# Kernel optimization log

Hardware: AMD Instinct MI355X
Metric: run time of the kernel (lower is better)

## Reference

```python
import jax, jax.numpy as jnp
import numpy as np

S, B, I, H = 256, 512, 46, 256  # seqlen, batch, i_dim, h_dim
EPS = 1e-5


def setup_inputs() -> dict:
    key = jax.random.key(0)
    ks = iter(jax.random.split(key, 64))
    nrm = lambda shape, s=0.05: jax.random.normal(next(ks), shape, dtype=jnp.float32) * s
    inp = {}
    inp['X'] = jax.random.normal(next(ks), (S, B, I), dtype=jnp.float32)
    inp['M'] = (jax.random.uniform(next(ks), (S, B, I)) > 0.5).astype(jnp.float32)
    inp['mask'] = (jax.random.uniform(next(ks), (S, B)) > 0.1).astype(jnp.float32)
    C = I - 6  # 40 clinical channels
    inp['i2h_w'] = nrm((H, 6)); inp['i2h_b'] = nrm((H,))
    inp['comb_w'] = nrm((C, 2 * C)); inp['comb_b'] = nrm((C,))
    inp['down_w'] = nrm((H, C)); inp['down_b'] = nrm((H,))
    inp['conv1_w'] = nrm((H, C)); inp['conv1_b'] = nrm((H,))
    inp['conv2_w'] = nrm((H, H)); inp['conv2_b'] = nrm((H,))
    inp['bn1_g'] = jnp.ones((H,), jnp.float32); inp['bn1_b'] = jnp.zeros((H,), jnp.float32)
    inp['bn2_g'] = jnp.ones((H,), jnp.float32); inp['bn2_b'] = jnp.zeros((H,), jnp.float32)
    for p in ('r1', 'r2'):
        inp[p + '_wih'] = nrm((3 * H, H)); inp[p + '_whh'] = nrm((3 * H, H))
        inp[p + '_bih'] = nrm((3 * H,)); inp[p + '_bhh'] = nrm((3 * H,))
        inp[p + '_cw'] = nrm((H, 2 * H)); inp[p + '_cb'] = nrm((H,))
    inp['ln1_g'] = jnp.ones((H,), jnp.float32); inp['ln1_b'] = jnp.zeros((H,), jnp.float32)
    inp['ln2_g'] = jnp.ones((H,), jnp.float32); inp['ln2_b'] = jnp.zeros((H,), jnp.float32)
    inp['ln3_g'] = jnp.ones((8,), jnp.float32); inp['ln3_b'] = jnp.zeros((8,), jnp.float32)
    inp['nn1_w'] = nrm((8, H)); inp['nn1_b'] = nrm((8,))
    inp['nn2_w'] = nrm((2, 8)); inp['nn2_b'] = nrm((2,))
    return inp


def _bn(x, g, b):
    # BatchNorm1d in training mode: stats over (seq, batch) per channel, biased var
    mu = x.mean((0, 1))
    var = x.var((0, 1))
    return (x - mu) * jax.lax.rsqrt(var + EPS) * g + b


def _ln(x, g, b):
    mu = x.mean(-1, keepdims=True)
    var = x.var(-1, keepdims=True)
    return (x - mu) * jax.lax.rsqrt(var + EPS) * g + b


def _modgru(Xs, h0, mask, wih, whh, bih, bhh, cw, cb):
    # precompute input-gate projections for all timesteps: [S,B,3H]
    gi = jnp.einsum('sbi,gi->sbg', Xs, wih) + bih

    def step(h, inp):
        x, g, m = inp  # x:[B,H], g:[B,3H], m:[B]
        gh = h @ whh.T + bhh
        ir, iz, inn = jnp.split(g, 3, axis=-1)
        hr, hz, hn = jnp.split(gh, 3, axis=-1)
        r = jax.nn.sigmoid(ir + hr)
        z = jax.nn.sigmoid(iz + hz)
        n = jnp.tanh(inn + r * hn)
        h_new = (1.0 - z) * n + z * h  # GRUCell update
        mm = m[:, None]
        h = h_new * mm + h * (1.0 - mm)  # mask blend
        out = jnp.concatenate([x, h], axis=-1) @ cw.T + cb  # com2
        return h, out

    _, outs = jax.lax.scan(step, h0, (Xs, gi, mask))
    return outs


def reference(X, M, mask, i2h_w, i2h_b, comb_w, comb_b, down_w, down_b,
              conv1_w, conv1_b, conv2_w, conv2_b, bn1_g, bn1_b, bn2_g, bn2_b,
              r1_wih, r1_whh, r1_bih, r1_bhh, r1_cw, r1_cb,
              r2_wih, r2_whh, r2_bih, r2_bhh, r2_cw, r2_cb,
              ln1_g, ln1_b, ln2_g, ln2_b, ln3_g, ln3_b,
              nn1_w, nn1_b, nn2_w, nn2_b):
    p_info = X[0, :, -6:]          # [B,6] static patient info
    Xin = X[:, :, :-6]             # [S,B,40]
    Min = M[:, :, :-6]
    h0 = p_info @ i2h_w.T + i2h_b  # [B,H]
    res = Xin @ down_w.T + down_b  # [S,B,H]
    Xc = jnp.concatenate([Xin, Min], axis=-1) @ comb_w.T + comb_b
    # kernel-size-1 convs == per-timestep linear (layout kept [S,B,C])
    out = Xc @ conv1_w.T + conv1_b
    out = jax.nn.relu(_bn(out, bn1_g, bn1_b))
    out = out @ conv2_w.T + conv2_b
    out = _bn(out, bn2_g, bn2_b)
    hx = out + res
    hx = _ln(_modgru(hx, h0, mask, r1_wih, r1_whh, r1_bih, r1_bhh, r1_cw, r1_cb), ln1_g, ln1_b)
    hx = _ln(_modgru(hx, h0, mask, r2_wih, r2_whh, r2_bih, r2_bhh, r2_cw, r2_cb), ln2_g, ln2_b)
    hx = jax.nn.relu(hx @ nn1_w.T + nn1_b)
    hx = _ln(hx, ln3_g, ln3_b)
    return hx @ nn2_w.T + nn2_b  # [S,B,2]
```

## Files before the change

### kernel.cpp

```cpp
#include <hip/hip_runtime.h>
#include <hip/hip_bf16.h>

#define SS 256
#define BB 512
#define II 46
#define HH 256
#define CC 40
#define SB (SS*BB)
#define G3 (3*HH)
#define EPSF 1e-5f
#define NPART (SB/64)

typedef __attribute__((ext_vector_type(8))) short bf16x8;
typedef __attribute__((ext_vector_type(4))) float f32x4;

__device__ __forceinline__ unsigned short f2bf_rne(float f){
  unsigned u = __float_as_uint(f);
  unsigned r = (u + 0x7FFFu + ((u >> 16) & 1u)) >> 16;
  return (unsigned short)r;
}
__device__ __forceinline__ float bf2f(unsigned short b){
  return __uint_as_float(((unsigned)b) << 16);
}
__device__ __forceinline__ void cvt8(const float* v, bf16x8& hi, bf16x8& lo){
  #pragma unroll
  for (int e=0;e<8;e++){
    unsigned short hb = f2bf_rne(v[e]);
    hi[e] = (short)hb;
    lo[e] = (short)f2bf_rne(v[e] - bf2f(hb));
  }
}

__global__ void split_w_k(const float* __restrict__ w, unsigned short* __restrict__ wh,
                          unsigned short* __restrict__ wl, int n){
  int i = blockIdx.x*256 + threadIdx.x;
  if (i >= n) return;
  float v = w[i];
  unsigned short hb = f2bf_rne(v);
  wh[i] = hb;
  wl[i] = f2bf_rne(v - bf2f(hb));
}

__global__ void h0_k(const float* __restrict__ X, const float* __restrict__ w,
                     const float* __restrict__ bias, float* __restrict__ h1c,
                     float* __restrict__ h2c){
  int b = blockIdx.x, jj = threadIdx.x;
  const float* p = X + (long long)b*II + (II - 6);
  float acc = bias[jj];
  #pragma unroll
  for (int c2=0;c2<6;c2++) acc = fmaf(p[c2], w[jj*6 + c2], acc);
  h1c[(long long)b*HH + jj] = acc;
  h2c[(long long)b*HH + jj] = acc;
}

__global__ void whht_bf_k(const float* __restrict__ w, unsigned short* __restrict__ wt){
  int idx = blockIdx.x*blockDim.x + threadIdx.x;
  if (idx >= G3*HH) return;
  int u = idx / HH, k = idx - u*HH;
  wt[(size_t)k*G3 + u] = f2bf_rne(w[idx]);
}

template<int MODE, int XM>
__global__ void gemm_tn(const float* __restrict__ A, int lda,
                        const float* __restrict__ W, int ldw,
                        const float* __restrict__ bias,
                        float* __restrict__ Co, int ldc,
                        int Mrows, int N, int K,
                        const float* __restrict__ A2, long long r0)
{
  __shared__ __align__(16) float As[32][132];
  __shared__ __align__(16) float Ws[32][132];
  const int m0 = blockIdx.x*128, n0 = blockIdx.y*128;
  const int t  = threadIdx.x;
  const int tm = t >> 4, tn = t & 15;
  float acc[8][8];
  #pragma unroll
  for (int i=0;i<8;i++)
    #pragma unroll
    for (int j2=0;j2<8;j2++) acc[i][j2] = 0.f;

  for (int k0=0;k0<K;k0+=32){
    #pragma unroll
    for (int u=0;u<16;u++){
      int idx = u*256 + t;
      int r = idx >> 5, c = idx & 31;
      int gk = k0 + c;
      float av = 0.f, wv = 0.f;
      if (gk < K){
        int gm = m0 + r;
        if (gm < Mrows){
          if (XM){
            long long gr = r0 + gm;
            av = (gk < CC) ? A[gr*II + gk] : A2[gr*II + (gk - CC)];
          } else {
            av = A[(long long)gm*lda + gk];
          }
        }
        int gn = n0 + r;
        if (gn < N)     wv = W[(long long)gn*ldw + gk];
      }
      As[c][r] = av;
      Ws[c][r] = wv;
    }
    __syncthreads();
    #pragma unroll
    for (int kk=0;kk<32;kk++){
      const float4 a0 = *(const float4*)&As[kk][tm*8];
      const float4 a1 = *(const float4*)&As[kk][tm*8+4];
      const float4 b0 = *(const float4*)&Ws[kk][tn*8];
      const float4 b1 = *(const float4*)&Ws[kk][tn*8+4];
      const float av[8] = {a0.x,a0.y,a0.z,a0.w,a1.x,a1.y,a1.z,a1.w};
      const float bv[8] = {b0.x,b0.y,b0.z,b0.w,b1.x,b1.y,b1.z,b1.w};
      #pragma unroll
      for (int i=0;i<8;i++)
        #pragma unroll
        for (int j2=0;j2<8;j2++) acc[i][j2] = fmaf(av[i], bv[j2], acc[i][j2]);
    }
    __syncthreads();
  }
  #pragma unroll
  for (int i=0;i<8;i++){
    int gm = m0 + tm*8 + i;
    if (gm < Mrows){
      #pragma unroll
      for (int j2=0;j2<8;j2++){
        int gn = n0 + tn*8 + j2;
        if (gn < N){
          long long oi = (long long)gm*ldc + gn;
          float val = acc[i][j2] + bias[gn];
          if (MODE == 1) val = fmaxf(val, 0.f);
          if (MODE == 2) val += Co[oi];
          Co[oi] = val;
        }
      }
    }
  }
}

__global__ void gemm_tn_dual2(const float* __restrict__ Xb, long long r0,
                              const float* __restrict__ W1, const float* __restrict__ b1,
                              float* __restrict__ Co1,
                              const float* __restrict__ A2, const float* __restrict__ W2,
                              const float* __restrict__ b2, float* __restrict__ Co2,
                              int Mrows)
{
  __shared__ __align__(16) float As1[32][132];
  __shared__ __align__(16) float As2[32][132];
  __shared__ __align__(16) float Ws1[32][132];
  __shared__ __align__(16) float Ws2[32][132];
  const int m0 = blockIdx.x*128, n0 = blockIdx.y*128;
  const int t  = threadIdx.x;
  const int tm = t >> 4, tn = t & 15;
  float acc1[8][8], acc2[8][8];
  #pragma unroll
  for (int i=0;i<8;i++)
    #pragma unroll
    for (int j2=0;j2<8;j2++){ acc1[i][j2] = 0.f; acc2[i][j2] = 0.f; }

  for (int k0=0;k0<CC;k0+=32){
    #pragma unroll
    for (int u=0;u<16;u++){
      int idx = u*256 + t;
      int r = idx >> 5, c = idx & 31;
      int gk = k0 + c;
      float a1=0.f, a2=0.f, w1=0.f, w2=0.f;
      if (gk < CC){
        int gm = m0 + r;
        if (gm < Mrows){
          long long gr = r0 + gm;
          a1 = Xb[gr*II + gk];
          a2 = A2[(long long)gm*CC + gk];
        }
        int gn = n0 + r;
        w1 = W1[(long long)gn*CC + gk];
        w2 = W2[(long long)gn*CC + gk];
      }
      As1[c][r] = a1; As2[c][r] = a2;
      Ws1[c][r] = w1; Ws2[c][r] = w2;
    }
    __syncthreads();
    #pragma unroll
    for (int kk=0;kk<32;kk++){
      const float4 p0 = *(const float4*)&As1[kk][tm*8];
      const float4 p1 = *(const float4*)&As1[kk][tm*8+4];
      const float4 q0 = *(const float4*)&As2[kk][tm*8];
      const float4 q1 = *(const float4*)&As2[kk][tm*8+4];
      const float4 u0 = *(const float4*)&Ws1[kk][tn*8];
      const float4 u1 = *(const float4*)&Ws1[kk][tn*8+4];
      const float4 v0 = *(const float4*)&Ws2[kk][tn*8];
      const float4 v1 = *(const float4*)&Ws2[kk][tn*8+4];
      const float a1v[8] = {p0.x,p0.y,p0.z,p0.w,p1.x,p1.y,p1.z,p1.w};
      const float a2v[8] = {q0.x,q0.y,q0.z,q0.w,q1.x,q1.y,q1.z,q1.w};
      const float w1v[8] = {u0.x,u0.y,u0.z,u0.w,u1.x,u1.y,u1.z,u1.w};
      const float w2v[8] = {v0.x,v0.y,v0.z,v0.w,v1.x,v1.y,v1.z,v1.w};
      #pragma unroll
      for (int i=0;i<8;i++)
        #pragma unroll
        for (int j2=0;j2<8;j2++){
          acc1[i][j2] = fmaf(a1v[i], w1v[j2], acc1[i][j2]);
          acc2[i][j2] = fmaf(a2v[i], w2v[j2], acc2[i][j2]);
        }
    }
    __syncthreads();
  }
  #pragma unroll
  for (int i=0;i<8;i++){
    int gm = m0 + tm*8 + i;
    if (gm < Mrows){
      #pragma unroll
      for (int j2=0;j2<8;j2++){
        int gn = n0 + tn*8 + j2;
        long long oi = (long long)gm*HH + gn;
        Co1[oi] = acc1[i][j2] + b1[gn];
        Co2[oi] = fmaxf(acc2[i][j2] + b2[gn], 0.f);
      }
    }
  }
}

template<int MODE>
__global__ __launch_bounds__(256) void gemm_mfp(
    const float* __restrict__ A, int lda,
    const unsigned short* __restrict__ Wh, const unsigned short* __restrict__ Wl, int ldw,
    const float* __restrict__ bias,
    float* __restrict__ Co, int ldc,
    int N, int K)
{
  __shared__ __align__(16) unsigned short Ah[128*32];
  __shared__ __align__(16) unsigned short Al[128*32];
  __shared__ __align__(16) unsigned short Bh[128*32];
  __shared__ __align__(16) unsigned short Bl[128*32];
  const int t = threadIdx.x;
  const int m0 = blockIdx.x*128, n0 = blockIdx.y*128;
  const int lane = t & 63, w = t >> 6;
  const int wm = (w & 1)*64, wn = (w >> 1)*64;
  const int fr = lane & 15, fg = lane >> 4;

  f32x4 acc[4][4];
  #pragma unroll
  for (int i=0;i<4;i++)
    #pragma unroll
    for (int j=0;j<4;j++){ f32x4 z; z[0]=0;z[1]=0;z[2]=0;z[3]=0; acc[i][j]=z; }

  for (int k0=0; k0<K; k0+=32){
    #pragma unroll
    for (int cc=0; cc<2; cc++){
      const int c   = t + cc*256;
      const int row = c >> 2, kg = c & 3;
      const int byte = row*64 + ((kg*16) ^ (((row>>1)&3)<<4));
      {
        const float* ap = A + (size_t)(m0+row)*lda + k0 + kg*8;
        float v[8];
        *(float4*)&v[0] = *(const float4*)ap;
        *(float4*)&v[4] = *(const float4*)(ap+4);
        bf16x8 hi, lo; cvt8(v, hi, lo);
        *(bf16x8*)((char*)Ah + byte) = hi;
        *(bf16x8*)((char*)Al + byte) = lo;
      }
      {
        const size_t off = (size_t)(n0+row)*ldw + k0 + kg*8;
        *(bf16x8*)((char*)Bh + byte) = *(const bf16x8*)&Wh[off];
        *(bf16x8*)((char*)Bl + byte) = *(const bf16x8*)&Wl[off];
      }
    }
    __syncthreads();
    bf16x8 ahi[4], alo[4], bhi[4], blo[4];
    #pragma unroll
    for (int mt=0; mt<4; mt++){
      const int r = wm + mt*16 + fr;
      const int byte = r*64 + ((fg*16) ^ (((r>>1)&3)<<4));
      ahi[mt] = *(const bf16x8*)((const char*)Ah + byte);
      alo[mt] = *(const bf16x8*)((const char*)Al + byte);
    }
    #pragma unroll
    for (int nt=0; nt<4; nt++){
      const int r = wn + nt*16 + fr;
      const int byte = r*64 + ((fg*16) ^ (((r>>1)&3)<<4));
      bhi[nt] = *(const bf16x8*)((const char*)Bh + byte);
      blo[nt] = *(const bf16x8*)((const char*)Bl + byte);
    }
    #pragma unroll
    for (int mt=0; mt<4; mt++)
      #pragma unroll
      for (int nt=0; nt<4; nt++){
        acc[mt][nt] = __builtin_amdgcn_mfma_f32_16x16x32_bf16(alo[mt], bhi[nt], acc[mt][nt], 0,0,0);
        acc[mt][nt] = __builtin_amdgcn_mfma_f32_16x16x32_bf16(ahi[mt], blo[nt], acc[mt][nt], 0,0,0);
        acc[mt][nt] = __builtin_amdgcn_mfma_f32_16x16x32_bf16(ahi[mt], bhi[nt], acc[mt][nt], 0,0,0);
      }
    __syncthreads();
  }

  #pragma unroll
  for (int mt=0; mt<4; mt++){
    #pragma unroll
    for (int nt=0; nt<4; nt++){
      const int col = n0 + wn + nt*16 + fr;
      const float bv = bias[col];
      #pragma unroll
      for (int i=0;i<4;i++){
        const int row = m0 + wm + mt*16 + fg*4 + i;
        const size_t oi = (size_t)row*ldc + col;
        float val = acc[mt][nt][i] + bv;
        if (MODE == 2) val += Co[oi];
        Co[oi] = val;
      }
    }
  }
}

__global__ __launch_bounds__(256) void gemm_mfp_dual(
    const float* __restrict__ A1, const float* __restrict__ A2,
    const unsigned short* __restrict__ Wh, const unsigned short* __restrict__ Wl,
    const float* __restrict__ bias,
    float* __restrict__ Co, int ldc, int N)
{
  __shared__ __align__(16) unsigned short Ah[128*32];
  __shared__ __align__(16) unsigned short Al[128*32];
  __shared__ __align__(16) unsigned short Bh[128*32];
  __shared__ __align__(16) unsigned short Bl[128*32];
  const int t = threadIdx.x;
  const int m0 = blockIdx.x*128, n0 = blockIdx.y*128;
  const int lane = t & 63, w = t >> 6;
  const int wm = (w & 1)*64, wn = (w >> 1)*64;
  const int fr = lane & 15, fg = lane >> 4;

  f32x4 acc[4][4];
  #pragma unroll
  for (int i=0;i<4;i++)
    #pragma unroll
    for (int j=0;j<4;j++){ f32x4 z; z[0]=0;z[1]=0;z[2]=0;z[3]=0; acc[i][j]=z; }

  for (int k0=0; k0<2*HH; k0+=32){
    const float* Abase = (k0 < HH) ? A1 : A2;
    const int    kofs  = (k0 < HH) ? k0 : (k0 - HH);
    #pragma unroll
    for (int cc=0; cc<2; cc++){
      const int c   = t + cc*256;
      const int row = c >> 2, kg = c & 3;
      const int byte = row*64 + ((kg*16) ^ (((row>>1)&3)<<4));
      {
        const float* ap = Abase + (size_t)(m0+row)*HH + kofs + kg*8;
        float v[8];
        *(float4*)&v[0] = *(const float4*)ap;
        *(float4*)&v[4] = *(const float4*)(ap+4);
        bf16x8 hi, lo; cvt8(v, hi, lo);
        *(bf16x8*)((char*)Ah + byte) = hi;
        *(bf16x8*)((char*)Al + byte) = lo;
      }
      {
        const size_t off = (size_t)(n0+row)*(2*HH) + k0 + kg*8;
        *(bf16x8*)((char*)Bh + byte) = *(const bf16x8*)&Wh[off];
        *(bf16x8*)((char*)Bl + byte) = *(const bf16x8*)&Wl[off];
      }
    }
    __syncthreads();
    bf16x8 ahi[4], alo[4], bhi[4], blo[4];
    #pragma unroll
    for (int mt=0; mt<4; mt++){
      const int r = wm + mt*16 + fr;
      const int byte = r*64 + ((fg*16) ^ (((r>>1)&3)<<4));
      ahi[mt] = *(const bf16x8*)((const char*)Ah + byte);
      alo[mt] = *(const bf16x8*)((const char*)Al + byte);
    }
    #pragma unroll
    for (int nt=0; nt<4; nt++){
      const int r = wn + nt*16 + fr;
      const int byte = r*64 + ((fg*16) ^ (((r>>1)&3)<<4));
      bhi[nt] = *(const bf16x8*)((const char*)Bh + byte);
      blo[nt] = *(const bf16x8*)((const char*)Bl + byte);
    }
    #pragma unroll
    for (int mt=0; mt<4; mt++)
      #pragma unroll
      for (int nt=0; nt<4; nt++){
        acc[mt][nt] = __builtin_amdgcn_mfma_f32_16x16x32_bf16(alo[mt], bhi[nt], acc[mt][nt], 0,0,0);
        acc[mt][nt] = __builtin_amdgcn_mfma_f32_16x16x32_bf16(ahi[mt], blo[nt], acc[mt][nt], 0,0,0);
        acc[mt][nt] = __builtin_amdgcn_mfma_f32_16x16x32_bf16(ahi[mt], bhi[nt], acc[mt][nt], 0,0,0);
      }
    __syncthreads();
  }

  #pragma unroll
  for (int mt=0; mt<4; mt++){
    #pragma unroll
    for (int nt=0; nt<4; nt++){
      const int col = n0 + wn + nt*16 + fr;
      const float bv = bias[col];
      #pragma unroll
      for (int i=0;i<4;i++){
        const int row = m0 + wm + mt*16 + fg*4 + i;
        const size_t oi = (size_t)row*ldc + col;
        Co[oi] = acc[mt][nt][i] + bv;
      }
    }
  }
}

__global__ void bn_partial_k(const float* __restrict__ Xc, float* __restrict__ ps,
                             float* __restrict__ pq, int pblk0){
  int blk = blockIdx.x, t = threadIdx.x;
  long long base = (long long)blk*64*HH;
  float s = 0.f, q = 0.f;
  for (int r=0;r<64;r++){
    float v = Xc[base + (long long)r*HH + t];
    s += v; q = fmaf(v, v, q);
  }
  ps[(size_t)(pblk0+blk)*HH + t] = s;
  pq[(size_t)(pblk0+blk)*HH + t] = q;
}

__global__ void bn_final_k(const float* __restrict__ ps, const float* __restrict__ pq,
                           const float* __restrict__ g, const float* __restrict__ b,
                           float* __restrict__ sc, float* __restrict__ sh){
  int t = threadIdx.x;
  double s = 0.0, q = 0.0;
  for (int i=0;i<NPART;i++){ s += (double)ps[(size_t)i*HH + t]; q += (double)pq[(size_t)i*HH + t]; }
  double mu  = s / (double)SB;
  double var = q / (double)SB - mu*mu;
  float scv = (float)((double)g[t] / sqrt(var + 1e-5));
  sc[t] = scv;
  sh[t] = (float)((double)b[t] - mu*(double)scv);
}

__global__ void fold_k(const float* __restrict__ w, const float* __restrict__ b,
                       const float* __restrict__ sc, const float* __restrict__ sh,
                       float* __restrict__ wf, float* __restrict__ bf, int K){
  int idx = blockIdx.x*blockDim.x + threadIdx.x;
  if (idx < 256*K){ int o = idx / K; wf[idx] = w[idx]*sc[o]; }
  if (idx < 256)  bf[idx] = b[idx]*sc[idx] + sh[idx];
}

__global__ void ln_rows_k(const float* __restrict__ Xi, float* __restrict__ Xo,
                          const float* __restrict__ g, const float* __restrict__ b){
  long long row = blockIdx.x;
  int t = threadIdx.x;
  float v = Xi[row*HH + t];
  float s = v, q = v*v;
  #pragma unroll
  for (int o=32;o>0;o>>=1){ s += __shfl_down(s,o); q += __shfl_down(q,o); }
  __shared__ float ssm[4], qqm[4];
  int w = t >> 6;
  if ((t & 63) == 0){ ssm[w] = s; qqm[w] = q; }
  __syncthreads();
  if (t == 0){ ssm[0] = ssm[0]+ssm[1]+ssm[2]+ssm[3]; qqm[0] = qqm[0]+qqm[1]+qqm[2]+qqm[3]; }
  __syncthreads();
  s = ssm[0]; q = qqm[0];
  float mu  = s * (1.f/HH);
  float var = q * (1.f/HH) - mu*mu;
  float rs  = rsqrtf(var + EPSF);
  Xo[row*HH + t] = (v - mu)*rs*g[t] + b[t];
}

#define DOT4(hv,A0,A1,A2,A3) \
  A0=fmaf(hv.x,w0.x,A0); A0=fmaf(hv.y,w1.x,A0); A0=fmaf(hv.z,w2.x,A0); A0=fmaf(hv.w,w3.x,A0); \
  A1=fmaf(hv.x,w0.y,A1); A1=fmaf(hv.y,w1.y,A1); A1=fmaf(hv.z,w2.y,A1); A1=fmaf(hv.w,w3.y,A1); \
  A2=fmaf(hv.x,w0.z,A2); A2=fmaf(hv.y,w1.z,A2); A2=fmaf(hv.z,w2.z,A2); A2=fmaf(hv.w,w3.z,A2); \
  A3=fmaf(hv.x,w0.w,A3); A3=fmaf(hv.y,w1.w,A3); A3=fmaf(hv.z,w2.w,A3); A3=fmaf(hv.w,w3.w,A3);

#define LDW_BF(dst, ofs) { \
  const uint2 u_ = *(const uint2*)(wbase + (size_t)(ofs)*G3); \
  dst.x = __uint_as_float(u_.x << 16); \
  dst.y = __uint_as_float(u_.x & 0xffff0000u); \
  dst.z = __uint_as_float(u_.y << 16); \
  dst.w = __uint_as_float(u_.y & 0xffff0000u); }

__global__ __launch_bounds__(768) void gru_scan_fused_k(
  const float* __restrict__ gi1, const unsigned short* __restrict__ w1T,
  const float* __restrict__ b1v, const float* __restrict__ m1v,
  float* __restrict__ hc1, float* __restrict__ Hh1o, int nst1,
  const float* __restrict__ gi2, const unsigned short* __restrict__ w2T,
  const float* __restrict__ b2v, const float* __restrict__ m2v,
  float* __restrict__ hc2, float* __restrict__ Hh2o, int nst2)
{
  const int gsel = blockIdx.x & 1;
  const int blk  = blockIdx.x >> 1;
  const float* gi    = gsel ? gi2 : gi1;
  const unsigned short* whhT = gsel ? w2T : w1T;
  const float* bhh   = gsel ? b2v : b1v;
  const float* mask0 = gsel ? m2v : m1v;
  float* hcar        = gsel ? hc2 : hc1;
  float* Hh          = gsel ? Hh2o : Hh1o;
  const int nst      = gsel ? nst2 : nst1;
  if (nst <= 0) return;

  const int t  = threadIdx.x;
  const int b0 = blk*4;
  const int cg = t % 192;
  const int ks = t / 192;
  const int c0 = cg*4;
  const int k0 = ks*64;
  __shared__ __align__(16) float h[4][260];
  __shared__ __align__(16) float part[4][4][776];
  __shared__ float mkz[4];

  const int uj = t & 255;
  const int ur = t >> 8;
  if (t < 512){
    h[ur  ][uj] = hcar[(size_t)(b0+ur  )*HH + uj];
    h[ur+2][uj] = hcar[(size_t)(b0+ur+2)*HH + uj];
  }
  float br=0.f, bz=0.f, bn_=0.f;
  if (t < 512){ br = bhh[uj]; bz = bhh[uj+HH]; bn_ = bhh[uj+2*HH]; }
  __syncthreads();

  const unsigned short* wbase = whhT + (size_t)k0*G3 + c0;

  for (int st=0; st<nst; ++st){
    float i0r=0,i0z=0,i0n=0, i1r=0,i1z=0,i1n=0;
    if (t < 512){
      const size_t ga = ((size_t)st*BB + b0 + ur  )*G3 + uj;
      const size_t gb = ((size_t)st*BB + b0 + ur+2)*G3 + uj;
      i0r=gi[ga]; i0z=gi[ga+HH]; i0n=gi[ga+2*HH];
      i1r=gi[gb]; i1z=gi[gb+HH]; i1n=gi[gb+2*HH];
    }
    if (t < 4) mkz[t] = mask0[(size_t)st*BB + b0 + t];

    float a00=0,a01=0,a02=0,a03=0;
    float a10=0,a11=0,a12=0,a13=0;
    float a20=0,a21=0,a22=0,a23=0;
    float a30=0,a31=0,a32=0,a33=0;
    #pragma unroll 4
    for (int kk=0; kk<64; kk+=4){
      float4 w0, w1, w2, w3;
      LDW_BF(w0, kk  );
      LDW_BF(w1, kk+1);
      LDW_BF(w2, kk+2);
      LDW_BF(w3, kk+3);
      const float4 h0 = *(const float4*)&h[0][k0+kk];
      const float4 h1 = *(const float4*)&h[1][k0+kk];
      const float4 h2 = *(const float4*)&h[2][k0+kk];
      const float4 h3 = *(const float4*)&h[3][k0+kk];
      DOT4(h0,a00,a01,a02,a03);
      DOT4(h1,a10,a11,a12,a13);
      DOT4(h2,a20,a21,a22,a23);
      DOT4(h3,a30,a31,a32,a33);
    }
    *(float4*)&part[ks][0][c0] = make_float4(a00,a01,a02,a03);
    *(float4*)&part[ks][1][c0] = make_float4(a10,a11,a12,a13);
    *(float4*)&part[ks][2][c0] = make_float4(a20,a21,a22,a23);
    *(float4*)&part[ks][3][c0] = make_float4(a30,a31,a32,a33);
    __syncthreads();

    if (t < 512){
      {
        const int r_ = ur;
        const float ar = part[0][r_][uj]+part[1][r_][uj]+part[2][r_][uj]+part[3][r_][uj] + br;
        const float az = part[0][r_][uj+HH]+part[1][r_][uj+HH]+part[2][r_][uj+HH]+part[3][r_][uj+HH] + bz;
        const float an = part[0][r_][uj+2*HH]+part[1][r_][uj+2*HH]+part[2][r_][uj+2*HH]+part[3][r_][uj+2*HH] + bn_;
        const float rr = 1.f/(1.f + __expf(-(i0r + ar)));
        const float zz = 1.f/(1.f + __expf(-(i0z + az)));
        const float nn = tanhf(fmaf(rr, an, i0n));
        const float hold = h[r_][uj];
        const float m = mkz[r_];
        const float hnew = (1.f - zz)*nn + zz*hold;
        const float hv = hnew*m + hold*(1.f - m);
        h[r_][uj] = hv;
        Hh[((size_t)st*BB + b0 + r_)*HH + uj] = hv;
      }
      {
        const int r_ = ur + 2;
        const float ar = part[0][r_][uj]+part[1][r_][uj]+part[2][r_][uj]+part[3][r_][uj] + br;
        const float az = part[0][r_][uj+HH]+part[1][r_][uj+HH]+part[2][r_][uj+HH]+part[3][r_][uj+HH] + bz;
        const float an = part[0][r_][uj+2*HH]+part[1][r_][uj+2*HH]+part[2][r_][uj+2*HH]+part[3][r_][uj+2*HH] + bn_;
        const float rr = 1.f/(1.f + __expf(-(i1r + ar)));
        const float zz = 1.f/(1.f + __expf(-(i1z + az)));
        const float nn = tanhf(fmaf(rr, an, i1n));
        const float hold = h[r_][uj];
        const float m = mkz[r_];
        const float hnew = (1.f - zz)*nn + zz*hold;
        const float hv = hnew*m + hold*(1.f - m);
        h[r_][uj] = hv;
        Hh[((size_t)st*BB + b0 + r_)*HH + uj] = hv;
      }
    }
    __syncthreads();
  }
  if (t < 512){
    hcar[(size_t)(b0+ur  )*HH + uj] = h[ur  ][uj];
    hcar[(size_t)(b0+ur+2)*HH + uj] = h[ur+2][uj];
  }
}

__global__ void head_ln_k(const float* __restrict__ hx,
                          const float* __restrict__ g2, const float* __restrict__ b2,
                          const float* __restrict__ w1, const float* __restrict__ b1,
                          const float* __restrict__ g3, const float* __restrict__ b3,
                          const float* __restrict__ w2, const float* __restrict__ b2h,
                          float* __restrict__ outp, long long r0){
  long long row = blockIdx.x;
  int t = threadIdx.x;
  float v = hx[row*HH + t];
  float s = v, q = v*v;
  #pragma unroll
  for (int o=32;o>0;o>>=1){ s += __shfl_down(s,o); q += __shfl_down(q,o); }
  __shared__ float ssm[4], qqm[4];
  int w = t >> 6;
  if ((t & 63) == 0){ ssm[w] = s; qqm[w] = q; }
  __syncthreads();
  if (t == 0){ ssm[0] = ssm[0]+ssm[1]+ssm[2]+ssm[3]; qqm[0] = qqm[0]+qqm[1]+qqm[2]+qqm[3]; }
  __syncthreads();
  s = ssm[0]; q = qqm[0];
  float mu  = s * (1.f/HH);
  float var = q * (1.f/HH) - mu*mu;
  float rs  = rsqrtf(var + EPSF);
  __shared__ float xs[HH];
  xs[t] = (v - mu)*rs*g2[t] + b2[t];
  __syncthreads();
  int o = t >> 5, l = t & 31;
  const float* wv = w1 + o*HH;
  float acc = 0.f;
  for (int k=l;k<HH;k+=32) acc = fmaf(xs[k], wv[k], acc);
  #pragma unroll
  for (int d=16;d>0;d>>=1) acc += __shfl_down(acc, d, 32);
  __shared__ float a8[8];
  if (l == 0) a8[o] = fmaxf(acc + b1[o], 0.f);
  __syncthreads();
  if (t == 0){
    float ss = 0.f;
    #pragma unroll
    for (int i=0;i<8;i++) ss += a8[i];
    float m8 = ss*0.125f;
    float qq = 0.f;
    #pragma unroll
    for (int i=0;i<8;i++){ float d = a8[i]-m8; qq = fmaf(d,d,qq); }
    float r8 = rsqrtf(qq*0.125f + EPSF);
    float y0 = b2h[0], y1 = b2h[1];
    #pragma unroll
    for (int i=0;i<8;i++){
      float vv = (a8[i]-m8)*r8*g3[i] + b3[i];
      y0 = fmaf(vv, w2[i],   y0);
      y1 = fmaf(vv, w2[8+i], y1);
    }
    outp[(r0+row)*2+0] = y0; outp[(r0+row)*2+1] = y1;
  }
}

extern "C" void kernel_launch(void* const* d_in, const int* in_sizes, int n_in,
                              void* d_out, int out_size, void* d_ws, size_t ws_size,
                              hipStream_t stream) {
  const float* X      = (const float*)d_in[0];
  const float* Mi     = (const float*)d_in[1];
  const float* mask   = (const float*)d_in[2];
  const float* i2h_w  = (const float*)d_in[3];
  const float* i2h_b  = (const float*)d_in[4];
  const float* comb_w = (const float*)d_in[5];
  const float* comb_b = (const float*)d_in[6];
  const float* down_w = (const float*)d_in[7];
  const float* down_b = (const float*)d_in[8];
  const float* conv1_w= (const float*)d_in[9];
  const float* conv1_b= (const float*)d_in[10];
  const float* conv2_w= (const float*)d_in[11];
  const float* conv2_b= (const float*)d_in[12];
  const float* bn1_g  = (const float*)d_in[13];
  const float* bn1_b  = (const float*)d_in[14];
  const float* bn2_g  = (const float*)d_in[15];
  const float* bn2_b  = (const float*)d_in[16];
  const float* r1_wih = (const float*)d_in[17];
  const float* r1_whh = (const float*)d_in[18];
  const float* r1_bih = (const float*)d_in[19];
  const float* r1_bhh = (const float*)d_in[20];
  const float* r1_cw  = (const float*)d_in[21];
  const float* r1_cb  = (const float*)d_in[22];
  const float* r2_wih = (const float*)d_in[23];
  const float* r2_whh = (const float*)d_in[24];
  const float* r2_bih = (const float*)d_in[25];
  const float* r2_bhh = (const float*)d_in[26];
  const float* r2_cw  = (const float*)d_in[27];
  const float* r2_cb  = (const float*)d_in[28];
  const float* ln1_g  = (const float*)d_in[29];
  const float* ln1_b  = (const float*)d_in[30];
  const float* ln2_g  = (const float*)d_in[31];
  const float* ln2_b  = (const float*)d_in[32];
  const float* ln3_g  = (const float*)d_in[33];
  const float* ln3_b  = (const float*)d_in[34];
  const float* nn1_w  = (const float*)d_in[35];
  const float* nn1_b  = (const float*)d_in[36];
  const float* nn2_w  = (const float*)d_in[37];
  const float* nn2_b  = (const float*)d_in[38];
  float* outp = (float*)d_out;

  const size_t us_elems = 2*((size_t)HH*HH + (size_t)HH*HH + (size_t)G3*HH
                           + (size_t)G3*HH + (size_t)HH*2*HH + (size_t)HH*2*HH)
                        + 2*(size_t)G3*HH;
  const size_t tail_floats = 2*(size_t)BB*HH + 2*(size_t)NPART*HH + 2*HH
                           + (size_t)256*40 + 256 + (size_t)HH*HH + 256
                           + (size_t)SB*CC
                           + (us_elems + 1)/2;
  int cands[6] = {256,128,64,32,16,8};
  int sc_chunk = 0;
  for (int ci=0; ci<6; ci++){
    size_t R = (size_t)512*cands[ci];
    size_t need = (R*2560 + tail_floats)*sizeof(float);
    if (need <= ws_size && R*2560 >= (size_t)SB*HH){ sc_chunk = cands[ci]; break; }
  }
  if (!sc_chunk) return;

  const size_t R = (size_t)512*sc_chunk;
  const int Ri = (int)R;
  const int nchunks = SB / Ri;

  float* wsf = (float*)d_ws;
  float* A   = wsf;
  float* GI1 = A + R*HH;
  float* Cxp = GI1;
  float* GI2 = GI1 + R*G3;
  float* Ee  = GI2 + R*G3;
  float* Hh2 = Ee + R*HH;
  float* Hx1 = Hh2 + R*HH;
  float* tl  = Hx1 + R*HH;
  float* H1C = tl;
  float* H2C = H1C + (size_t)BB*HH;
  float* PS  = H2C + (size_t)BB*HH;
  float* PQ  = PS  + (size_t)NPART*HH;
  float* SCv = PQ  + (size_t)NPART*HH;
  float* SHv = SCv + HH;
  float* W1F = SHv + HH;
  float* B1F = W1F + (size_t)256*40;
  float* W2F = B1F + HH;
  float* B2F = W2F + (size_t)HH*HH;
  float* XcF = B2F + HH;
  unsigned short* usb = (unsigned short*)(XcF + (size_t)SB*CC);
  unsigned short* C2H  = usb;
  unsigned short* C2L  = C2H  + (size_t)HH*HH;
  unsigned short* W2FH = C2L  + (size_t)HH*HH;
  unsigned short* W2FL = W2FH + (size_t)HH*HH;
  unsigned short* WI1H = W2FL + (size_t)HH*HH;
  unsigned short* WI1L = WI1H + (size_t)G3*HH;
  unsigned short* WI2H = WI1L + (size_t)G3*HH;
  unsigned short* WI2L = WI2H + (size_t)G3*HH;
  unsigned short* CW1H = WI2L + (size_t)G3*HH;
  unsigned short* CW1L = CW1H + (size_t)HH*2*HH;
  unsigned short* CW2H = CW1L + (size_t)HH*2*HH;
  unsigned short* CW2L = CW2H + (size_t)HH*2*HH;
  unsigned short* W1Tb = CW2L + (size_t)HH*2*HH;
  unsigned short* W2Tb = W1Tb + (size_t)HH*G3;

  whht_bf_k<<<(G3*HH + 255)/256, 256, 0, stream>>>(r1_whh, W1Tb);
  whht_bf_k<<<(G3*HH + 255)/256, 256, 0, stream>>>(r2_whh, W2Tb);
  split_w_k<<<(HH*HH + 255)/256, 256, 0, stream>>>(conv2_w, C2H, C2L, HH*HH);
  split_w_k<<<(G3*HH + 255)/256, 256, 0, stream>>>(r1_wih, WI1H, WI1L, G3*HH);
  split_w_k<<<(G3*HH + 255)/256, 256, 0, stream>>>(r2_wih, WI2H, WI2L, G3*HH);
  split_w_k<<<(HH*2*HH + 255)/256, 256, 0, stream>>>(r1_cw, CW1H, CW1L, HH*2*HH);
  split_w_k<<<(HH*2*HH + 255)/256, 256, 0, stream>>>(r2_cw, CW2H, CW2L, HH*2*HH);

  const int MB = Ri/128;

  {
    float* SA = wsf;
    gemm_tn<0,1><<<dim3(SB/128,1), 256, 0, stream>>>(X, II, comb_w, 80, comb_b, XcF, CC, SB, CC, 80, Mi, 0);
    gemm_tn<0,0><<<dim3(SB/128,2), 256, 0, stream>>>(XcF, CC, conv1_w, CC, conv1_b, SA, HH, SB, HH, CC, nullptr, 0);
    bn_partial_k<<<SB/64, 256, 0, stream>>>(SA, PS, PQ, 0);
  }
  bn_final_k<<<1, 256, 0, stream>>>(PS, PQ, bn1_g, bn1_b, SCv, SHv);
  fold_k<<<(256*40 + 255)/256, 256, 0, stream>>>(conv1_w, conv1_b, SCv, SHv, W1F, B1F, 40);

  {
    float* SA2 = wsf;
    float* SB2 = wsf + (size_t)(SB/2)*HH;
    for (int hlf=0; hlf<2; hlf++){
      long long r0 = (long long)hlf*(SB/2);
      gemm_tn<1,0><<<dim3(SB/256,2), 256, 0, stream>>>(XcF + r0*CC, CC, W1F, CC, B1F, SA2, HH, SB/2, HH, CC, nullptr, 0);
      gemm_mfp<0><<<dim3(SB/256,2), 256, 0, stream>>>(SA2, HH, C2H, C2L, HH, conv2_b, SB2, HH, HH, HH);
      bn_partial_k<<<(SB/2)/64, 256, 0, stream>>>(SB2, PS, PQ, (int)(r0/64));
    }
  }
  bn_final_k<<<1, 256, 0, stream>>>(PS, PQ, bn2_g, bn2_b, SCv, SHv);
  fold_k<<<(256*256 + 255)/256, 256, 0, stream>>>(conv2_w, conv2_b, SCv, SHv, W2F, B2F, 256);
  split_w_k<<<(HH*HH + 255)/256, 256, 0, stream>>>(W2F, W2FH, W2FL, HH*HH);

  h0_k<<<BB, HH, 0, stream>>>(X, i2h_w, i2h_b, H1C, H2C);

  for (int c=0;c<nchunks;c++){
    long long r0 = (long long)c*R;
    long long rp = r0 - (long long)R;
    gemm_tn_dual2<<<dim3(MB,2), 256, 0, stream>>>(X, r0, down_w, down_b, A,
                                                  XcF + r0*CC, W1F, B1F, Ee, Ri);
    gemm_mfp<2><<<dim3(MB,2), 256, 0, stream>>>(Ee, HH, W2FH, W2FL, HH, B2F, A, HH, HH, HH);
    gemm_mfp<0><<<dim3(MB,6), 256, 0, stream>>>(A, HH, WI1H, WI1L, HH, r1_bih, GI1, G3, G3, HH);
    gru_scan_fused_k<<<2*(BB/4), 768, 0, stream>>>(
        GI1, W1Tb, r1_bhh, mask + r0, H1C, Ee, sc_chunk,
        GI2, W2Tb, r2_bhh, (c > 0) ? (mask + rp) : mask, H2C, Hh2, (c > 0) ? sc_chunk : 0);
    if (c > 0){
      gemm_mfp_dual<<<dim3(MB,2), 256, 0, stream>>>(Hx1, Hh2, CW2H, CW2L, r2_cb, Cxp, HH, HH);
      head_ln_k<<<Ri, 256, 0, stream>>>(Cxp, ln2_g, ln2_b, nn1_w, nn1_b, ln3_g, ln3_b, nn2_w, nn2_b, outp, rp);
    }
    gemm_mfp_dual<<<dim3(MB,2), 256, 0, stream>>>(A, Ee, CW1H, CW1L, r1_cb, Cxp, HH, HH);
    ln_rows_k<<<Ri, 256, 0, stream>>>(Cxp, Hx1, ln1_g, ln1_b);
    gemm_mfp<0><<<dim3(MB,6), 256, 0, stream>>>(Hx1, HH, WI2H, WI2L, HH, r2_bih, GI2, G3, G3, HH);
  }
  {
    long long rl = (long long)(nchunks-1)*R;
    gru_scan_fused_k<<<2*(BB/4), 768, 0, stream>>>(
        GI1, W1Tb, r1_bhh, mask, H1C, Ee, 0,
        GI2, W2Tb, r2_bhh, mask + rl, H2C, Hh2, sc_chunk);
    gemm_mfp_dual<<<dim3(MB,2), 256, 0, stream>>>(Hx1, Hh2, CW2H, CW2L, r2_cb, Cxp, HH, HH);
    head_ln_k<<<Ri, 256, 0, stream>>>(Cxp, ln2_g, ln2_b, nn1_w, nn1_b, ln3_g, ln3_b, nn2_w, nn2_b, outp, rl);
  }
}
```

Before: 6.456 ms.

## Compute GRU recurrent matvec with bf16 MFMA and split-precision hidden state

Replaces the scalar FMA recurrent h·Whh product in the GRU scan with 16x16x32 bf16 MFMA instructions. Whh is pre-packed into per-lane fragment layout. The hidden state is split into hi/lo bf16 parts in LDS so the product keeps near-fp32 accuracy, with the weights still single bf16. The block shrinks to 512 threads and the cross-warp partial-sum reduction is dropped. Only 4 of the 16 MFMA rows carry real batch rows, so most of the matrix work is padding, and the bf16 fragment loads still come from global/L2 every step.

```diff
diff --git a/kernel.cpp b/kernel.cpp
--- a/kernel.cpp
+++ b/kernel.cpp
@@ -53,11 +53,16 @@
   h2c[(long long)b*HH + jj] = acc;
 }
 
-__global__ void whht_bf_k(const float* __restrict__ w, unsigned short* __restrict__ wt){
-  int idx = blockIdx.x*blockDim.x + threadIdx.x;
-  if (idx >= G3*HH) return;
-  int u = idx / HH, k = idx - u*HH;
-  wt[(size_t)k*G3 + u] = f2bf_rne(w[idx]);
+__global__ void wfrag_k(const float* __restrict__ whh, unsigned short* __restrict__ wf){
+  int tid = blockIdx.x*256 + threadIdx.x;
+  if (tid >= 384*64) return;
+  int f = tid >> 6, l = tid & 63;
+  int ntile = f >> 3, kt = f & 7;
+  int col = ntile*16 + (l & 15);
+  int k0  = kt*32 + (l >> 4)*8;
+  unsigned short* dst = wf + (((size_t)f)*64 + l)*8;
+  #pragma unroll
+  for (int e=0;e<8;e++) dst[e] = f2bf_rne(whh[(size_t)col*HH + k0 + e]);
 }
 
 template<int MODE, int XM>
@@ -451,31 +456,18 @@
   Xo[row*HH + t] = (v - mu)*rs*g[t] + b[t];
 }
 
-#define DOT4(hv,A0,A1,A2,A3) \
-  A0=fmaf(hv.x,w0.x,A0); A0=fmaf(hv.y,w1.x,A0); A0=fmaf(hv.z,w2.x,A0); A0=fmaf(hv.w,w3.x,A0); \
-  A1=fmaf(hv.x,w0.y,A1); A1=fmaf(hv.y,w1.y,A1); A1=fmaf(hv.z,w2.y,A1); A1=fmaf(hv.w,w3.y,A1); \
-  A2=fmaf(hv.x,w0.z,A2); A2=fmaf(hv.y,w1.z,A2); A2=fmaf(hv.z,w2.z,A2); A2=fmaf(hv.w,w3.z,A2); \
-  A3=fmaf(hv.x,w0.w,A3); A3=fmaf(hv.y,w1.w,A3); A3=fmaf(hv.z,w2.w,A3); A3=fmaf(hv.w,w3.w,A3);
-
-#define LDW_BF(dst, ofs) { \
-  const uint2 u_ = *(const uint2*)(wbase + (size_t)(ofs)*G3); \
-  dst.x = __uint_as_float(u_.x << 16); \
-  dst.y = __uint_as_float(u_.x & 0xffff0000u); \
-  dst.z = __uint_as_float(u_.y << 16); \
-  dst.w = __uint_as_float(u_.y & 0xffff0000u); }
-
-__global__ __launch_bounds__(768) void gru_scan_fused_k(
-  const float* __restrict__ gi1, const unsigned short* __restrict__ w1T,
+__global__ __launch_bounds__(512) void gru_scan_mfma_k(
+  const float* __restrict__ gi1, const unsigned short* __restrict__ wf1,
   const float* __restrict__ b1v, const float* __restrict__ m1v,
   float* __restrict__ hc1, float* __restrict__ Hh1o, int nst1,
-  const float* __restrict__ gi2, const unsigned short* __restrict__ w2T,
+  const float* __restrict__ gi2, const unsigned short* __restrict__ wf2,
   const float* __restrict__ b2v, const float* __restrict__ m2v,
   float* __restrict__ hc2, float* __restrict__ Hh2o, int nst2)
 {
   const int gsel = blockIdx.x & 1;
   const int blk  = blockIdx.x >> 1;
   const float* gi    = gsel ? gi2 : gi1;
-  const unsigned short* whhT = gsel ? w2T : w1T;
+  const unsigned short* wfr = gsel ? wf2 : wf1;
   const float* bhh   = gsel ? b2v : b1v;
   const float* mask0 = gsel ? m2v : m1v;
   float* hcar        = gsel ? hc2 : hc1;
@@ -483,102 +475,105 @@
   const int nst      = gsel ? nst2 : nst1;
   if (nst <= 0) return;
 
-  const int t  = threadIdx.x;
-  const int b0 = blk*4;
-  const int cg = t % 192;
-  const int ks = t / 192;
-  const int c0 = cg*4;
-  const int k0 = ks*64;
-  __shared__ __align__(16) float h[4][260];
-  __shared__ __align__(16) float part[4][4][776];
+  const int t    = threadIdx.x;
+  const int b0   = blk*4;
+  const int lane = t & 63, wid = t >> 6;
+  const int arow = lane & 15, kg = lane >> 4;
+  const bool act = (arow < 4);
+  const int uj = t & 255, ur = t >> 8;
+
+  __shared__ __align__(16) unsigned short AhS[4][256];
+  __shared__ __align__(16) unsigned short AlS[4][256];
+  __shared__ __align__(16) float ghS[4][768];
   __shared__ float mkz[4];
 
-  const int uj = t & 255;
-  const int ur = t >> 8;
-  if (t < 512){
-    h[ur  ][uj] = hcar[(size_t)(b0+ur  )*HH + uj];
-    h[ur+2][uj] = hcar[(size_t)(b0+ur+2)*HH + uj];
-  }
-  float br=0.f, bz=0.f, bn_=0.f;
-  if (t < 512){ br = bhh[uj]; bz = bhh[uj+HH]; bn_ = bhh[uj+2*HH]; }
+  float hold0 = hcar[(size_t)(b0+ur  )*HH + uj];
+  float hold1 = hcar[(size_t)(b0+ur+2)*HH + uj];
+  const float br = bhh[uj], bz = bhh[uj+HH], bn_ = bhh[uj+2*HH];
+
+  {
+    unsigned short hb0 = f2bf_rne(hold0);
+    AhS[ur  ][uj] = hb0;  AlS[ur  ][uj] = f2bf_rne(hold0 - bf2f(hb0));
+    unsigned short hb1 = f2bf_rne(hold1);
+    AhS[ur+2][uj] = hb1;  AlS[ur+2][uj] = f2bf_rne(hold1 - bf2f(hb1));
+  }
   __syncthreads();
 
-  const unsigned short* wbase = whhT + (size_t)k0*G3 + c0;
+  const unsigned short* wfbase = wfr + (((size_t)(wid*6)*8)*64 + lane)*8;
 
   for (int st=0; st<nst; ++st){
-    float i0r=0,i0z=0,i0n=0, i1r=0,i1z=0,i1n=0;
-    if (t < 512){
-      const size_t ga = ((size_t)st*BB + b0 + ur  )*G3 + uj;
-      const size_t gb = ((size_t)st*BB + b0 + ur+2)*G3 + uj;
-      i0r=gi[ga]; i0z=gi[ga+HH]; i0n=gi[ga+2*HH];
-      i1r=gi[gb]; i1z=gi[gb+HH]; i1n=gi[gb+2*HH];
-    }
+    const size_t ga = ((size_t)st*BB + b0 + ur  )*G3 + uj;
+    const size_t gb = ((size_t)st*BB + b0 + ur+2)*G3 + uj;
+    const float i0r=gi[ga], i0z=gi[ga+HH], i0n=gi[ga+2*HH];
+    const float i1r=gi[gb], i1z=gi[gb+HH], i1n=gi[gb+2*HH];
     if (t < 4) mkz[t] = mask0[(size_t)st*BB + b0 + t];
 
-    float a00=0,a01=0,a02=0,a03=0;
-    float a10=0,a11=0,a12=0,a13=0;
-    float a20=0,a21=0,a22=0,a23=0;
-    float a30=0,a31=0,a32=0,a33=0;
-    #pragma unroll 4
-    for (int kk=0; kk<64; kk+=4){
-      float4 w0, w1, w2, w3;
-      LDW_BF(w0, kk  );
-      LDW_BF(w1, kk+1);
-      LDW_BF(w2, kk+2);
-      LDW_BF(w3, kk+3);
-      const float4 h0 = *(const float4*)&h[0][k0+kk];
-      const float4 h1 = *(const float4*)&h[1][k0+kk];
-      const float4 h2 = *(const float4*)&h[2][k0+kk];
-      const float4 h3 = *(const float4*)&h[3][k0+kk];
-      DOT4(h0,a00,a01,a02,a03);
-      DOT4(h1,a10,a11,a12,a13);
-      DOT4(h2,a20,a21,a22,a23);
-      DOT4(h3,a30,a31,a32,a33);
-    }
-    *(float4*)&part[ks][0][c0] = make_float4(a00,a01,a02,a03);
-    *(float4*)&part[ks][1][c0] = make_float4(a10,a11,a12,a13);
-    *(float4*)&part[ks][2][c0] = make_float4(a20,a21,a22,a23);
-    *(float4*)&part[ks][3][c0] = make_float4(a30,a31,a32,a33);
-    __syncthreads();
-
-    if (t < 512){
-      {
-        const int r_ = ur;
-        const float ar = part[0][r_][uj]+part[1][r_][uj]+part[2][r_][uj]+part[3][r_][uj] + br;
-        const float az = part[0][r_][uj+HH]+part[1][r_][uj+HH]+part[2][r_][uj+HH]+part[3][r_][uj+HH] + bz;
-        const float an = part[0][r_][uj+2*HH]+part[1][r_][uj+2*HH]+part[2][r_][uj+2*HH]+part[3][r_][uj+2*HH] + bn_;
-        const float rr = 1.f/(1.f + __expf(-(i0r + ar)));
-        const float zz = 1.f/(1.f + __expf(-(i0z + az)));
-        const float nn = tanhf(fmaf(rr, an, i0n));
-        const float hold = h[r_][uj];
-        const float m = mkz[r_];
-        const float hnew = (1.f - zz)*nn + zz*hold;
-        const float hv = hnew*m + hold*(1.f - m);
-        h[r_][uj] = hv;
-        Hh[((size_t)st*BB + b0 + r_)*HH + uj] = hv;
-      }
-      {
-        const int r_ = ur + 2;
-        const float ar = part[0][r_][uj]+part[1][r_][uj]+part[2][r_][uj]+part[3][r_][uj] + br;
-        const float az = part[0][r_][uj+HH]+part[1][r_][uj+HH]+part[2][r_][uj+HH]+part[3][r_][uj+HH] + bz;
-        const float an = part[0][r_][uj+2*HH]+part[1][r_][uj+2*HH]+part[2][r_][uj+2*HH]+part[3][r_][uj+2*HH] + bn_;
-        const float rr = 1.f/(1.f + __expf(-(i1r + ar)));
-        const float zz = 1.f/(1.f + __expf(-(i1z + az)));
-        const float nn = tanhf(fmaf(rr, an, i1n));
-        const float hold = h[r_][uj];
-        const float m = mkz[r_];
-        const float hnew = (1.f - zz)*nn + zz*hold;
-        const float hv = hnew*m + hold*(1.f - m);
-        h[r_][uj] = hv;
-        Hh[((size_t)st*BB + b0 + r_)*HH + uj] = hv;
-      }
-    }
-    __syncthreads();
-  }
-  if (t < 512){
-    hcar[(size_t)(b0+ur  )*HH + uj] = h[ur  ][uj];
-    hcar[(size_t)(b0+ur+2)*HH + uj] = h[ur+2][uj];
-  }
+    bf16x8 AH[8], AL[8];
+    #pragma unroll
+    for (int kt=0; kt<8; kt++){
+      if (act){
+        AH[kt] = *(const bf16x8*)&AhS[arow][kt*32 + kg*8];
+        AL[kt] = *(const bf16x8*)&AlS[arow][kt*32 + kg*8];
+      } else {
+        bf16x8 z = {0,0,0,0,0,0,0,0};
+        AH[kt] = z; AL[kt] = z;
+      }
+    }
+    #pragma unroll
+    for (int nt=0; nt<6; nt++){
+      const unsigned short* wp = wfbase + (size_t)nt*8*64*8;
+      f32x4 acc = {0.f,0.f,0.f,0.f};
+      #pragma unroll
+      for (int kt=0; kt<8; kt++){
+        const bf16x8 b = *(const bf16x8*)(wp + (size_t)kt*64*8);
+        acc = __builtin_amdgcn_mfma_f32_16x16x32_bf16(AL[kt], b, acc, 0,0,0);
+        acc = __builtin_amdgcn_mfma_f32_16x16x32_bf16(AH[kt], b, acc, 0,0,0);
+      }
+      if (lane < 16){
+        const int col = (wid*6 + nt)*16 + lane;
+        ghS[0][col] = acc[0];
+        ghS[1][col] = acc[1];
+        ghS[2][col] = acc[2];
+        ghS[3][col] = acc[3];
+      }
+    }
+    __syncthreads();
+
+    {
+      const float ar = ghS[ur][uj]       + br;
+      const float az = ghS[ur][uj+HH]    + bz;
+      const float an = ghS[ur][uj+2*HH]  + bn_;
+      const float rr = 1.f/(1.f + __expf(-(i0r + ar)));
+      const float zz = 1.f/(1.f + __expf(-(i0z + az)));
+      const float nn = tanhf(fmaf(rr, an, i0n));
+      const float m  = mkz[ur];
+      const float hnew = (1.f - zz)*nn + zz*hold0;
+      const float hv = hnew*m + hold0*(1.f - m);
+      hold0 = hv;
+      unsigned short hb = f2bf_rne(hv);
+      AhS[ur][uj] = hb; AlS[ur][uj] = f2bf_rne(hv - bf2f(hb));
+      Hh[((size_t)st*BB + b0 + ur)*HH + uj] = hv;
+    }
+    {
+      const int r_ = ur + 2;
+      const float ar = ghS[r_][uj]       + br;
+      const float az = ghS[r_][uj+HH]    + bz;
+      const float an = ghS[r_][uj+2*HH]  + bn_;
+      const float rr = 1.f/(1.f + __expf(-(i1r + ar)));
+      const float zz = 1.f/(1.f + __expf(-(i1z + az)));
+      const float nn = tanhf(fmaf(rr, an, i1n));
+      const float m  = mkz[r_];
+      const float hnew = (1.f - zz)*nn + zz*hold1;
+      const float hv = hnew*m + hold1*(1.f - m);
+      hold1 = hv;
+      unsigned short hb = f2bf_rne(hv);
+      AhS[r_][uj] = hb; AlS[r_][uj] = f2bf_rne(hv - bf2f(hb));
+      Hh[((size_t)st*BB + b0 + r_)*HH + uj] = hv;
+    }
+    __syncthreads();
+  }
+  hcar[(size_t)(b0+ur  )*HH + uj] = hold0;
+  hcar[(size_t)(b0+ur+2)*HH + uj] = hold1;
 }
 
 __global__ void head_ln_k(const float* __restrict__ hx,
@@ -732,11 +727,11 @@
   unsigned short* CW1L = CW1H + (size_t)HH*2*HH;
   unsigned short* CW2H = CW1L + (size_t)HH*2*HH;
   unsigned short* CW2L = CW2H + (size_t)HH*2*HH;
-  unsigned short* W1Tb = CW2L + (size_t)HH*2*HH;
-  unsigned short* W2Tb = W1Tb + (size_t)HH*G3;
-
-  whht_bf_k<<<(G3*HH + 255)/256, 256, 0, stream>>>(r1_whh, W1Tb);
-  whht_bf_k<<<(G3*HH + 255)/256, 256, 0, stream>>>(r2_whh, W2Tb);
+  unsigned short* WF1  = CW2L + (size_t)HH*2*HH;
+  unsigned short* WF2  = WF1 + (size_t)G3*HH;
+
+  wfrag_k<<<(384*64 + 255)/256, 256, 0, stream>>>(r1_whh, WF1);
+  wfrag_k<<<(384*64 + 255)/256, 256, 0, stream>>>(r2_whh, WF2);
   split_w_k<<<(HH*HH + 255)/256, 256, 0, stream>>>(conv2_w, C2H, C2L, HH*HH);
   split_w_k<<<(G3*HH + 255)/256, 256, 0, stream>>>(r1_wih, WI1H, WI1L, G3*HH);
   split_w_k<<<(G3*HH + 255)/256, 256, 0, stream>>>(r2_wih, WI2H, WI2L, G3*HH);
@@ -777,9 +772,9 @@
                                                   XcF + r0*CC, W1F, B1F, Ee, Ri);
     gemm_mfp<2><<<dim3(MB,2), 256, 0, stream>>>(Ee, HH, W2FH, W2FL, HH, B2F, A, HH, HH, HH);
     gemm_mfp<0><<<dim3(MB,6), 256, 0, stream>>>(A, HH, WI1H, WI1L, HH, r1_bih, GI1, G3, G3, HH);
-    gru_scan_fused_k<<<2*(BB/4), 768, 0, stream>>>(
-        GI1, W1Tb, r1_bhh, mask + r0, H1C, Ee, sc_chunk,
-        GI2, W2Tb, r2_bhh, (c > 0) ? (mask + rp) : mask, H2C, Hh2, (c > 0) ? sc_chunk : 0);
+    gru_scan_mfma_k<<<2*(BB/4), 512, 0, stream>>>(
+        GI1, WF1, r1_bhh, mask + r0, H1C, Ee, sc_chunk,
+        GI2, WF2, r2_bhh, (c > 0) ? (mask + rp) : mask, H2C, Hh2, (c > 0) ? sc_chunk : 0);
     if (c > 0){
       gemm_mfp_dual<<<dim3(MB,2), 256, 0, stream>>>(Hx1, Hh2, CW2H, CW2L, r2_cb, Cxp, HH, HH);
       head_ln_k<<<Ri, 256, 0, stream>>>(Cxp, ln2_g, ln2_b, nn1_w, nn1_b, ln3_g, ln3_b, nn2_w, nn2_b, outp, rp);
@@ -790,9 +785,9 @@
   }
   {
     long long rl = (long long)(nchunks-1)*R;
-    gru_scan_fused_k<<<2*(BB/4), 768, 0, stream>>>(
-        GI1, W1Tb, r1_bhh, mask, H1C, Ee, 0,
-        GI2, W2Tb, r2_bhh, mask + rl, H2C, Hh2, sc_chunk);
+    gru_scan_mfma_k<<<2*(BB/4), 512, 0, stream>>>(
+        GI1, WF1, r1_bhh, mask, H1C, Ee, 0,
+        GI2, WF2, r2_bhh, mask + rl, H2C, Hh2, sc_chunk);
     gemm_mfp_dual<<<dim3(MB,2), 256, 0, stream>>>(Hx1, Hh2, CW2H, CW2L, r2_cb, Cxp, HH, HH);
     head_ln_k<<<Ri, 256, 0, stream>>>(Cxp, ln2_g, ln2_b, nn1_w, nn1_b, ln3_g, ln3_b, nn2_w, nn2_b, outp, rl);
   }
```

Result: faster. 5.903 ms (-8.6%).
